# Performance work log

Hardware: AMD Instinct MI355X
Metric: run time of the kernel (lower is better)

Reference implementation:

```python
import jax, jax.numpy as jnp
import numpy as np

N_SIGMA = 1
NUM_CLASS = 1
N_INST = 16          # max instance id (ids 1..16); instances==0 is background
W_INST, W_VAR, W_SEED = 1.0, 10.0, 1.0
H, W, B = 512, 512, 8
GRID = 1024          # buffer is linspace over 1024 then cropped to H,W


def make_xym(h, w, dtype=jnp.float32):
    full = jnp.linspace(0.0, 1.0, GRID, dtype=dtype)
    xm = jnp.broadcast_to(full[:w][None, :], (h, w))   # x varies along width
    ym = jnp.broadcast_to(full[:h][:, None], (h, w))   # y varies along height
    return jnp.stack([xm, ym], axis=0)                 # [2, H, W]


def lovasz_hinge_flat(logits, labels):
    # logits: [N] float, labels: [N] float in {0,1}
    signs = 2.0 * labels - 1.0
    errors = 1.0 - logits * signs
    order = jnp.argsort(-errors)
    errors_sorted = errors[order]
    gt_sorted = labels[order]
    gts = jnp.sum(gt_sorted)
    intersection = gts - jnp.cumsum(gt_sorted)
    union = gts + jnp.cumsum(1.0 - gt_sorted)
    jaccard = 1.0 - intersection / union
    grad = jnp.concatenate([jaccard[:1], jaccard[1:] - jaccard[:-1]])
    return jnp.sum(jax.nn.relu(errors_sorted) * grad)


def _per_image(pred, instance, label, xym):
    h, w = pred.shape[1], pred.shape[2]
    spatial_emb = jnp.tanh(pred[0:2]) + xym              # [2,H,W]
    sigma = pred[2:2 + N_SIGMA]                          # [n_sigma,H,W]
    seed = jax.nn.sigmoid(pred[2 + N_SIGMA])             # [H,W] (num_class==1)

    label_mask = (label == 1)
    bg_mask = (label == 0)
    seed_loss = jnp.sum(jnp.where(bg_mask, seed ** 2, 0.0))

    ids = jnp.arange(1, N_INST + 1)
    masks = (instance[None] == ids[:, None, None]) & label_mask[None]  # [K,H,W] bool
    maskf = masks.astype(pred.dtype)
    counts = jnp.sum(maskf, axis=(1, 2))                 # [K]
    present = counts > 0
    safe = jnp.maximum(counts, 1.0)

    # to_center=True: center = mean of xym coords over each instance mask
    center = jnp.einsum('khw,chw->kc', maskf, xym) / safe[:, None]        # [K,2]
    s_mean = jnp.einsum('khw,shw->ks', maskf, sigma) / safe[:, None]      # [K,n_sigma]

    # var loss: mean over in-mask pixels of (sigma - detached mean)^2
    dev2 = (sigma[None] - jax.lax.stop_gradient(s_mean)[:, :, None, None]) ** 2  # [K,ns,H,W]
    var_terms = jnp.einsum('khw,kshw->k', maskf, dev2) / (safe * N_SIGMA)

    # dist = exp(-s * sum_c (emb_c - center_c)^2), s = exp(10 * mean sigma)
    s_exp = jnp.exp(10.0 * s_mean)[:, 0]                 # [K] (n_sigma==1 broadcasts)
    diff2 = jnp.sum((spatial_emb[None] - center[:, :, None, None]) ** 2, axis=1)  # [K,H,W]
    dist = jnp.exp(-s_exp[:, None, None] * diff2)        # [K,H,W]

    inst_losses = jax.vmap(
        lambda d, m: lovasz_hinge_flat(2.0 * d.ravel() - 1.0, m.ravel())
    )(dist, maskf)
    instance_loss = jnp.sum(jnp.where(present, inst_losses, 0.0))
    var_loss = jnp.sum(jnp.where(present, var_terms, 0.0))

    seed_loss = seed_loss + jnp.sum(
        maskf * (seed[None] - jax.lax.stop_gradient(dist)) ** 2)

    obj = jnp.maximum(jnp.sum(present.astype(pred.dtype)), 1.0)
    return (W_INST * instance_loss / obj
            + W_VAR * var_loss / obj
            + W_SEED * seed_loss / (h * w))


def setup_inputs() -> dict:
    key = jax.random.key(0)
    k1, k2, k3 = jax.random.split(key, 3)
    prediction = jax.random.normal(k1, (B, 2 + N_SIGMA + NUM_CLASS, H, W), dtype=jnp.float32)
    instances = jax.random.randint(k2, (B, H, W), 0, N_INST + 1).astype(jnp.int64)
    labels = jax.random.randint(k3, (B, H, W), 0, NUM_CLASS + 1).astype(jnp.int64)
    return {"prediction": prediction, "instances": instances, "labels": labels}


def reference(prediction, instances, labels):
    xym = make_xym(prediction.shape[2], prediction.shape[3], prediction.dtype)
    per_img = jax.vmap(_per_image, in_axes=(0, 0, 0, None))(
        prediction, instances, labels, xym)
    return jnp.mean(per_img)
```

## Files before the change

kernel.cpp:

```cpp
#include <hip/hip_runtime.h>
#include <math.h>

#define HWPX 262144
#define NIMG 8
#define ACC_STRIDE 96
#define NB 512
#define ZMAX 8.0f
#define NSPLIT 64
#define PREP_GRID 2048

typedef unsigned long long u64;

__device__ __forceinline__ float tanh_fast(float x) {
  float t = __expf(2.0f * x);
  return 1.0f - __fdividef(2.0f, t + 1.0f);
}
__device__ __forceinline__ float sigmoid_fast(float x) {
  return __fdividef(1.0f, 1.0f + __expf(-x));
}

__global__ __launch_bounds__(256) void k_stats(const float* __restrict__ pred,
    const int* __restrict__ inst, const int* __restrict__ lab,
    float* __restrict__ part)
{
  __shared__ float s[8][83];
  int t = threadIdx.x;
  for (int i = t; i < 8*83; i += 256) (&s[0][0])[i] = 0.0f;
  __syncthreads();
  int bid = blockIdx.x;
  int b = bid >> 8;
  int px0 = ((bid & 255) << 10) + t*4;
  const float* pb = pred + (size_t)b*4*HWPX;
  size_t ib = (size_t)b*HWPX;
  int r = t & 7;
  int w0 = px0 & 511;
  float ym = (float)(px0 >> 9) * (1.0f/1023.0f);

  float4 Gv = *(const float4*)(pb + 2*HWPX + px0);
  float4 Q  = *(const float4*)(pb + 3*HWPX + px0);
  int4   L  = *(const int4*)(lab + ib + px0);
  int4   I  = *(const int4*)(inst + ib + px0);

  float bg = 0.0f;
#define PXS(C, GG, QQ, LL, II) { \
    float xm = (float)(w0 + C) * (1.0f/1023.0f); \
    int mid = ((LL) == 1 && (unsigned)((II)-1) < 16u) ? (II) : 0; \
    if ((LL) == 0) { float sd = sigmoid_fast(QQ); bg += sd*sd; } \
    else if (mid) { int k = mid - 1; \
      atomicAdd(&s[r][k], 1.0f); \
      atomicAdd(&s[r][16+k], xm); \
      atomicAdd(&s[r][32+k], ym); \
      atomicAdd(&s[r][48+k], GG); \
      atomicAdd(&s[r][64+k], (GG)*(GG)); } }
  PXS(0, Gv.x, Q.x, L.x, I.x)
  PXS(1, Gv.y, Q.y, L.y, I.y)
  PXS(2, Gv.z, Q.z, L.z, I.z)
  PXS(3, Gv.w, Q.w, L.w, I.w)
#undef PXS

  #pragma unroll
  for (int o = 32; o > 0; o >>= 1) bg += __shfl_down(bg, o);
  if ((t & 63) == 0) atomicAdd(&s[0][80], bg);
  __syncthreads();
  if (t < 96) {
    float v = 0.0f;
    if (t < 83) {
      #pragma unroll
      for (int rr = 0; rr < 8; ++rr) v += s[rr][t];
    }
    part[(size_t)bid*96 + t] = v;
  }
}

__global__ __launch_bounds__(1024) void k_fin(const float* __restrict__ part,
    double* __restrict__ accd, float* __restrict__ pairinfo)
{
  __shared__ float red2[10*96];
  int t = threadIdx.x, b = blockIdx.x;
  if (t < 960) {
    int e = t % 96, c = t / 96;
    int lo = c*26, hi = lo + 26; if (hi > 256) hi = 256;
    const float* pp = part + (size_t)b*256*96 + e;
    float v = 0.0f;
    for (int blk = lo; blk < hi; ++blk) v += pp[(size_t)blk*96];
    red2[c*96 + e] = v;
  }
  __syncthreads();
  if (t < 96) {
    float v = 0.0f;
    #pragma unroll
    for (int cc = 0; cc < 10; ++cc) v += red2[cc*96 + t];
    red2[t] = v;
  }
  __syncthreads();
  if (t < 16) {
    float cnt = red2[t];
    float safe = cnt > 0.0f ? cnt : 1.0f;
    float sm = red2[48+t] / safe;
    float4 pi = make_float4(red2[16+t]/safe, red2[32+t]/safe, __expf(10.0f*sm), cnt);
    ((float4*)pairinfo)[b*16 + t] = pi;
  }
  if (t == 0) {
    double vs = 0.0; float np = 0.0f;
    for (int k2 = 0; k2 < 16; ++k2) {
      float cnt = red2[k2];
      if (cnt > 0.0f) {
        np += 1.0f;
        float ssg = red2[48+k2];
        float var = (red2[64+k2] - ssg*ssg/cnt) / cnt;
        if (var < 0.0f) var = 0.0f;
        vs += (double)var;
      }
    }
    double* ab = accd + (size_t)b*ACC_STRIDE;
    ab[80] = (double)red2[80];
    ab[81] = 0.0;
    ab[82] = 0.0;
    ab[83] = vs;
    ab[84] = np > 1.0f ? (double)np : 1.0;
  }
}

__global__ __launch_bounds__(1024, 4) void k_hist(const float* __restrict__ pred,
    const int* __restrict__ inst, const int* __restrict__ lab,
    const float* __restrict__ pairinfo,
    unsigned* __restrict__ partial, double* __restrict__ accd)
{
  __shared__ unsigned hist[16*NB];
  __shared__ float redf[16];
  int t = threadIdx.x, bid = blockIdx.x;
  int b = bid & 7;
  int s = bid >> 3;
  for (int i = t; i < 16*NB; i += 1024) hist[i] = 0u;
  float cx[16], cy[16], s128[16];
  #pragma unroll
  for (int j = 0; j < 16; ++j) {
    float4 pi = ((const float4*)pairinfo)[b*16 + j];
    cx[j] = pi.x; cy[j] = pi.y; s128[j] = pi.z * (float)(NB/ZMAX);
  }
  __syncthreads();
  int px0 = s*(HWPX/NSPLIT) + t*4;
  const float* pb = pred + (size_t)b*4*HWPX;
  size_t ib = (size_t)b*HWPX;
  float4 X = *(const float4*)(pb + px0);
  float4 Y = *(const float4*)(pb + HWPX + px0);
  float4 Q = *(const float4*)(pb + 3*HWPX + px0);
  int4   L = *(const int4*)(lab + ib + px0);
  int4   I = *(const int4*)(inst + ib + px0);
  int w0 = px0 & 511;
  float ym = (float)(px0 >> 9) * (1.0f/1023.0f);
  float fit = 0.0f;

#define PXH(C, XX, YY, QQ, LL, II) { \
    float xm = (float)(w0 + C) * (1.0f/1023.0f); \
    float exf = tanh_fast(XX) + xm; \
    float eyf = tanh_fast(YY) + ym; \
    float sd = sigmoid_fast(QQ); \
    int rel = ((LL) == 1 && (unsigned)((II)-1) < 16u) ? ((II)-1) : -1; \
    _Pragma("unroll") \
    for (int j = 0; j < 16; ++j) { \
      float dx = exf - cx[j], dy = eyf - cy[j]; \
      float z = fmaf(dx, dx, dy*dy) * s128[j]; \
      float d = __expf(-z * (ZMAX/(float)NB)); \
      bool m = (j == rel); \
      float e = fmaf(-2.0f, d, 2.0f); \
      int kp = (int)(e * (float)(NB/2)); kp = kp > NB-1 ? NB-1 : kp; \
      int kn = (int)fminf(z, (float)(NB-1)); \
      atomicAdd(&hist[j*NB + (m ? kp : kn)], m ? 0x10000u : 1u); \
      if (m) { float df = sd - d; fit += df*df; } \
    } }
  PXH(0, X.x, Y.x, Q.x, L.x, I.x)
  PXH(1, X.y, Y.y, Q.y, L.y, I.y)
  PXH(2, X.z, Y.z, Q.z, L.z, I.z)
  PXH(3, X.w, Y.w, Q.w, L.w, I.w)
#undef PXH

  #pragma unroll
  for (int o = 32; o > 0; o >>= 1) fit += __shfl_down(fit, o);
  if ((t & 63) == 0) redf[t >> 6] = fit;
  __syncthreads();
  if (t == 0) {
    float ft = 0.0f;
    for (int i = 0; i < 16; ++i) ft += redf[i];
    atomicAdd(&accd[(size_t)b*ACC_STRIDE + 81], (double)ft);
  }
  unsigned* pp = partial + (size_t)(b*NSPLIT + s)*(16*NB);
  for (int i = t; i < 16*NB; i += 1024) pp[i] = hist[i];
}

__global__ __launch_bounds__(512) void k_scan(const unsigned* __restrict__ partial,
    const float* __restrict__ pairinfo, double* __restrict__ accd)
{
  __shared__ unsigned sp[NB], sq[NB];
  __shared__ float red[8];
  int t = threadIdx.x, bid = blockIdx.x;
  int b = bid >> 4, k = bid & 15;
  float G = pairinfo[(b*16 + k)*4 + 3];
  if (G <= 0.0f) return;
  sq[t] = 0u;
  __syncthreads();
  unsigned p = 0, q = 0;
  const unsigned* basep = partial + (size_t)(b*NSPLIT)*(16*NB) + k*NB + t;
  #pragma unroll 4
  for (int s2 = 0; s2 < NSPLIT; ++s2) {
    unsigned h = basep[(size_t)s2*(16*NB)];
    p += h >> 16; q += h & 0xffffu;
  }
  float zmid = (t + 0.5f) * (ZMAX/NB);
  float ev = 2.0f * __expf(-zmid);
  int eb = (int)(ev * (float)(NB/2));
  if (eb > NB-1) eb = NB-1;
  if (q) atomicAdd(&sq[eb], q);
  __syncthreads();
  unsigned qe = sq[t];
  __syncthreads();
  int j = (NB-1) - t;
  sp[j] = p; sq[j] = qe;
  __syncthreads();
  for (int off = 1; off < NB; off <<= 1) {
    unsigned vp = 0, vq = 0;
    if (j >= off) { vp = sp[j-off]; vq = sq[j-off]; }
    __syncthreads();
    sp[j] += vp; sq[j] += vq;
    __syncthreads();
  }
  float A  = (float)(sp[j] - p);
  float Bn = (float)(sq[j] - qe);
  float val = (t + 0.5f) * (2.0f/NB);
  float pf = (float)p, qf = (float)qe;
  float Jb = (A + Bn) / (G + Bn);
  float Ja = (A + Bn + pf + qf) / (G + Bn + qf);
  float contrib = val * (Ja - Jb);
  #pragma unroll
  for (int o = 32; o > 0; o >>= 1) contrib += __shfl_down(contrib, o);
  if ((t & 63) == 0) red[t >> 6] = contrib;
  __syncthreads();
  if (t == 0) {
    float tot = 0.0f;
    for (int i = 0; i < 8; ++i) tot += red[i];
    atomicAdd(&accd[(size_t)b*ACC_STRIDE + 82], (double)tot);
  }
}

__global__ __launch_bounds__(1024) void k_lov_old(const float* __restrict__ pred,
    const int* __restrict__ inst, const int* __restrict__ lab,
    const float* __restrict__ pairinfo, double* __restrict__ accd)
{
  constexpr int SHIFT = 18;
  constexpr int NBB = (0x40000000 >> SHIFT) + 1;
  extern __shared__ unsigned char smem[];
  unsigned* histP = reinterpret_cast<unsigned*>(smem);
  unsigned* histQ = histP + NBB;
  unsigned* scanP = histQ + NBB;
  unsigned* scanQ = scanP + 1024;
  float* red  = reinterpret_cast<float*>(scanQ + 1024);
  float* redf = red + 16;
  int t = threadIdx.x, bid = blockIdx.x;
  int b = bid >> 4, k = bid & 15;
  float4 pi = reinterpret_cast<const float4*>(pairinfo)[bid];
  float cx = pi.x, cy = pi.y, sexp = pi.z, G = pi.w;
  if (G <= 0.0f) return;
  for (int i = t; i < 2*NBB; i += 1024) histP[i] = 0u;
  __syncthreads();
  size_t ib = (size_t)b * HWPX;
  const float* pb = pred + (size_t)b * 4 * HWPX;
  const int target = k + 1;
  float fit = 0.0f;
  for (int j = 0; j < HWPX/1024; ++j) {
    int px = (j << 10) + t;
    int h = px >> 9, w = px & 511;
    float ex = tanhf(pb[px]) + w*(1.0f/1023.0f);
    float ey = tanhf(pb[HWPX+px]) + h*(1.0f/1023.0f);
    float sd = 1.0f/(1.0f + __expf(-pb[3*HWPX+px]));
    int lv = lab[ib+px], iv = inst[ib+px];
    float dx = ex - cx, dy = ey - cy;
    float d = __expf(-sexp * (dx*dx + dy*dy));
    bool m = (lv == 1) && (iv == target);
    float e = m ? fmaf(-2.0f, d, 2.0f) : 2.0f * d;
    unsigned key = __float_as_uint(e) >> SHIFT;
    atomicAdd(m ? &histP[key] : &histQ[key], 1u);
    if (m) { float df = sd - d; fit += df*df; }
  }
  #pragma unroll
  for (int o = 32; o > 0; o >>= 1) fit += __shfl_down(fit, o);
  if ((t & 63) == 0) redf[t >> 6] = fit;
  __syncthreads();
  constexpr int CB = NBB / 1024;
  int start = (NBB - 1) - t * CB;
  int nk = (t == 1023) ? (CB + 1) : CB;
  unsigned lp = 0, lq = 0;
  for (int i = 0; i < nk; ++i) { lp += histP[start-i]; lq += histQ[start-i]; }
  scanP[t] = lp; scanQ[t] = lq;
  __syncthreads();
  for (int off = 1; off < 1024; off <<= 1) {
    unsigned vp = 0, vq = 0;
    if (t >= off) { vp = scanP[t-off]; vq = scanQ[t-off]; }
    __syncthreads();
    scanP[t] += vp; scanQ[t] += vq;
    __syncthreads();
  }
  float A  = (float)(scanP[t] - lp);
  float Bn = (float)(scanQ[t] - lq);
  float contrib = 0.0f;
  for (int i = 0; i < nk; ++i) {
    int kk = start - i;
    unsigned p = histP[kk], q = histQ[kk];
    if (p | q) {
      float lo = __uint_as_float((unsigned)kk << SHIFT);
      float hi = __uint_as_float((unsigned)(kk+1) << SHIFT);
      float valv = 0.5f*(lo+hi);
      if (valv > 2.0f) valv = 2.0f;
      float pq = (float)(p + q), qf = (float)q;
      float Jb = (A + Bn) / (G + Bn);
      float Ja = (A + Bn + pq) / (G + Bn + qf);
      contrib += valv * (Ja - Jb);
      A += (float)p; Bn += qf;
    }
  }
  #pragma unroll
  for (int o = 32; o > 0; o >>= 1) contrib += __shfl_down(contrib, o);
  if ((t & 63) == 0) red[t >> 6] = contrib;
  __syncthreads();
  if (t == 0) {
    float tot = 0.0f, ft = 0.0f;
    for (int i = 0; i < 16; ++i) { tot += red[i]; ft += redf[i]; }
    atomicAdd(&accd[(size_t)b*ACC_STRIDE + 82], (double)tot);
    atomicAdd(&accd[(size_t)b*ACC_STRIDE + 81], (double)ft);
  }
}

__global__ void k_final(const double* __restrict__ accd, float* __restrict__ out)
{
  int t = threadIdx.x;
  double lb = 0.0;
  if (t < NIMG) {
    const double* ab = accd + (size_t)t*ACC_STRIDE;
    lb = (ab[82] + 10.0*ab[83]) / ab[84] + (ab[80] + ab[81]) * (1.0/(double)HWPX);
  }
  #pragma unroll
  for (int o = 4; o > 0; o >>= 1) lb += __shfl_down(lb, o);
  if (t == 0) out[0] = (float)(lb * 0.125);
}

extern "C" void kernel_launch(void* const* d_in, const int* in_sizes, int n_in,
                              void* d_out, int out_size, void* d_ws, size_t ws_size,
                              hipStream_t stream)
{
  const float* pred = (const float*)d_in[0];
  const int*   inst = (const int*)d_in[1];
  const int*   lab  = (const int*)d_in[2];
  float* out = (float*)d_out;

  size_t partB  = (size_t)NIMG * NSPLIT * 16 * NB * 4;
  size_t pstatB = (size_t)PREP_GRID * 96 * sizeof(float);
  size_t accB   = (size_t)NIMG * ACC_STRIDE * sizeof(double);
  size_t pairB  = 128 * 4 * sizeof(float);
  bool full = ws_size >= partB + pstatB + accB + pairB;

  char* ws = (char*)d_ws;
  if (full) {
    unsigned* part  = (unsigned*)ws;
    float*    pstat = (float*)(ws + partB);
    double*   accd  = (double*)(ws + partB + pstatB);
    float*    pairinfo = (float*)(ws + partB + pstatB + accB);
    k_stats<<<PREP_GRID,256,0,stream>>>(pred, inst, lab, pstat);
    k_fin<<<NIMG,1024,0,stream>>>(pstat, accd, pairinfo);
    k_hist<<<NIMG*NSPLIT,1024,0,stream>>>(pred, inst, lab, pairinfo, part, accd);
    k_scan<<<128,512,0,stream>>>(part, pairinfo, accd);
    k_final<<<1,64,0,stream>>>(accd, out);
  } else {
    float*    pstat = (float*)ws;
    double*   accd  = (double*)(ws + pstatB);
    float*    pairinfo = (float*)(ws + pstatB + accB);
    k_stats<<<PREP_GRID,256,0,stream>>>(pred, inst, lab, pstat);
    k_fin<<<NIMG,1024,0,stream>>>(pstat, accd, pairinfo);
    size_t lds18 = ((size_t)2*4097 + 2048)*4 + 128;
    k_lov_old<<<128,1024,lds18,stream>>>(pred, inst, lab, pairinfo, accd);
    k_final<<<1,64,0,stream>>>(accd, out);
  }
}
```

Before: 81.75 us.

## Pack seed and instance id in stats pass, slim histogram kernel, fuse final reduction

The stats kernel now writes a packed per-pixel word holding the fp16 seed sigmoid and the valid instance id. The histogram kernel reads that word instead of the seed, label and instance arrays. The histogram kernel uses 256-thread blocks that each process 16 pixels per thread, and it evaluates the exponential only for the pixel's own instance. The final reduction moves into the scan kernel through a last-block ticket counter, which removes one launch. This adds an 8 MB intermediate write, fp16 rounding of the seed value, and reliance on the ticket counter's initial state.

```diff
diff --git a/kernel.cpp b/kernel.cpp
--- a/kernel.cpp
+++ b/kernel.cpp
@@ -1,4 +1,5 @@
 #include <hip/hip_runtime.h>
+#include <hip/hip_fp16.h>
 #include <math.h>
 
 #define HWPX 262144
@@ -7,7 +8,7 @@
 #define NB 512
 #define ZMAX 8.0f
 #define NSPLIT 64
-#define PREP_GRID 2048
+#define STAT_GRID 2048
 
 typedef unsigned long long u64;
 
@@ -19,9 +20,10 @@
   return __fdividef(1.0f, 1.0f + __expf(-x));
 }
 
+template<bool PACK>
 __global__ __launch_bounds__(256) void k_stats(const float* __restrict__ pred,
     const int* __restrict__ inst, const int* __restrict__ lab,
-    float* __restrict__ part)
+    unsigned* __restrict__ meta, float* __restrict__ part)
 {
   __shared__ float s[8][83];
   int t = threadIdx.x;
@@ -42,21 +44,27 @@
   int4   I  = *(const int4*)(inst + ib + px0);
 
   float bg = 0.0f;
-#define PXS(C, GG, QQ, LL, II) { \
+  unsigned m0=0,m1=0,m2=0,m3=0;
+#define PXS(MV, C, GG, QQ, LL, II) { \
     float xm = (float)(w0 + C) * (1.0f/1023.0f); \
+    float sd = sigmoid_fast(QQ); \
     int mid = ((LL) == 1 && (unsigned)((II)-1) < 16u) ? (II) : 0; \
-    if ((LL) == 0) { float sd = sigmoid_fast(QQ); bg += sd*sd; } \
+    if (PACK) MV = ((unsigned)__half_as_ushort(__float2half(sd)) << 16) | (unsigned)mid; \
+    if ((LL) == 0) { bg += sd*sd; } \
     else if (mid) { int k = mid - 1; \
       atomicAdd(&s[r][k], 1.0f); \
       atomicAdd(&s[r][16+k], xm); \
       atomicAdd(&s[r][32+k], ym); \
       atomicAdd(&s[r][48+k], GG); \
       atomicAdd(&s[r][64+k], (GG)*(GG)); } }
-  PXS(0, Gv.x, Q.x, L.x, I.x)
-  PXS(1, Gv.y, Q.y, L.y, I.y)
-  PXS(2, Gv.z, Q.z, L.z, I.z)
-  PXS(3, Gv.w, Q.w, L.w, I.w)
+  PXS(m0, 0, Gv.x, Q.x, L.x, I.x)
+  PXS(m1, 1, Gv.y, Q.y, L.y, I.y)
+  PXS(m2, 2, Gv.z, Q.z, L.z, I.z)
+  PXS(m3, 3, Gv.w, Q.w, L.w, I.w)
 #undef PXS
+  if (PACK) {
+    *(uint4*)(meta + ib + px0) = make_uint4(m0, m1, m2, m3);
+  }
 
   #pragma unroll
   for (int o = 32; o > 0; o >>= 1) bg += __shfl_down(bg, o);
@@ -121,124 +129,154 @@
   }
 }
 
-__global__ __launch_bounds__(1024, 4) void k_hist(const float* __restrict__ pred,
-    const int* __restrict__ inst, const int* __restrict__ lab,
-    const float* __restrict__ pairinfo,
+__global__ __launch_bounds__(256) void k_hist(const float* __restrict__ pred,
+    const unsigned* __restrict__ meta, const float* __restrict__ pairinfo,
     unsigned* __restrict__ partial, double* __restrict__ accd)
 {
   __shared__ unsigned hist[16*NB];
-  __shared__ float redf[16];
+  __shared__ float redf[4];
   int t = threadIdx.x, bid = blockIdx.x;
   int b = bid & 7;
   int s = bid >> 3;
-  for (int i = t; i < 16*NB; i += 1024) hist[i] = 0u;
+  for (int i = t; i < 16*NB; i += 256) hist[i] = 0u;
   float cx[16], cy[16], s128[16];
   #pragma unroll
   for (int j = 0; j < 16; ++j) {
     float4 pi = ((const float4*)pairinfo)[b*16 + j];
-    cx[j] = pi.x; cy[j] = pi.y; s128[j] = pi.z * (float)(NB/ZMAX);
-  }
-  __syncthreads();
-  int px0 = s*(HWPX/NSPLIT) + t*4;
+    cx[j] = pi.x; cy[j] = pi.y; s128[j] = pi.z * ((float)NB/ZMAX);
+  }
+  __syncthreads();
+  int px0 = s*(HWPX/NSPLIT) + t*16;
   const float* pb = pred + (size_t)b*4*HWPX;
   size_t ib = (size_t)b*HWPX;
-  float4 X = *(const float4*)(pb + px0);
-  float4 Y = *(const float4*)(pb + HWPX + px0);
-  float4 Q = *(const float4*)(pb + 3*HWPX + px0);
-  int4   L = *(const int4*)(lab + ib + px0);
-  int4   I = *(const int4*)(inst + ib + px0);
-  int w0 = px0 & 511;
+  int wbase = px0 & 511;
   float ym = (float)(px0 >> 9) * (1.0f/1023.0f);
   float fit = 0.0f;
 
-#define PXH(C, XX, YY, QQ, LL, II) { \
-    float xm = (float)(w0 + C) * (1.0f/1023.0f); \
+  for (int it4 = 0; it4 < 4; ++it4) {
+    int px = px0 + it4*4;
+    float4 X = *(const float4*)(pb + px);
+    float4 Y = *(const float4*)(pb + HWPX + px);
+    uint4  M = *(const uint4*)(meta + ib + px);
+    int wb = wbase + it4*4;
+#define PXH(C, XX, YY, MM) { \
+    float xm = (float)(wb + C) * (1.0f/1023.0f); \
     float exf = tanh_fast(XX) + xm; \
     float eyf = tanh_fast(YY) + ym; \
-    float sd = sigmoid_fast(QQ); \
-    int rel = ((LL) == 1 && (unsigned)((II)-1) < 16u) ? ((II)-1) : -1; \
+    int rel = (int)((MM) & 0xffu) - 1; \
+    float sd = __half2float(__ushort_as_half((unsigned short)((MM) >> 16))); \
     _Pragma("unroll") \
     for (int j = 0; j < 16; ++j) { \
       float dx = exf - cx[j], dy = eyf - cy[j]; \
       float z = fmaf(dx, dx, dy*dy) * s128[j]; \
-      float d = __expf(-z * (ZMAX/(float)NB)); \
-      bool m = (j == rel); \
-      float e = fmaf(-2.0f, d, 2.0f); \
-      int kp = (int)(e * (float)(NB/2)); kp = kp > NB-1 ? NB-1 : kp; \
-      int kn = (int)fminf(z, (float)(NB-1)); \
-      atomicAdd(&hist[j*NB + (m ? kp : kn)], m ? 0x10000u : 1u); \
-      if (m) { float df = sd - d; fit += df*df; } \
+      int key; unsigned add; \
+      if (j == rel) { \
+        float d = __expf(-z * (ZMAX/(float)NB)); \
+        float e = fmaf(-2.0f, d, 2.0f); \
+        int kp = (int)(e * (float)(NB/2)); key = kp > NB-1 ? NB-1 : kp; \
+        add = 0x10000u; \
+        float df = sd - d; fit += df*df; \
+      } else { \
+        key = (int)fminf(z, (float)(NB-1)); \
+        add = 1u; \
+      } \
+      atomicAdd(&hist[j*NB + key], add); \
     } }
-  PXH(0, X.x, Y.x, Q.x, L.x, I.x)
-  PXH(1, X.y, Y.y, Q.y, L.y, I.y)
-  PXH(2, X.z, Y.z, Q.z, L.z, I.z)
-  PXH(3, X.w, Y.w, Q.w, L.w, I.w)
+    PXH(0, X.x, Y.x, M.x)
+    PXH(1, X.y, Y.y, M.y)
+    PXH(2, X.z, Y.z, M.z)
+    PXH(3, X.w, Y.w, M.w)
 #undef PXH
+  }
 
   #pragma unroll
   for (int o = 32; o > 0; o >>= 1) fit += __shfl_down(fit, o);
   if ((t & 63) == 0) redf[t >> 6] = fit;
   __syncthreads();
   if (t == 0) {
-    float ft = 0.0f;
-    for (int i = 0; i < 16; ++i) ft += redf[i];
+    float ft = redf[0] + redf[1] + redf[2] + redf[3];
     atomicAdd(&accd[(size_t)b*ACC_STRIDE + 81], (double)ft);
   }
   unsigned* pp = partial + (size_t)(b*NSPLIT + s)*(16*NB);
-  for (int i = t; i < 16*NB; i += 1024) pp[i] = hist[i];
+  for (int i = t; i < 16*NB; i += 256) pp[i] = hist[i];
 }
 
 __global__ __launch_bounds__(512) void k_scan(const unsigned* __restrict__ partial,
-    const float* __restrict__ pairinfo, double* __restrict__ accd)
+    const float* __restrict__ pairinfo, double* __restrict__ accd,
+    float* __restrict__ out, unsigned* __restrict__ tick)
 {
   __shared__ unsigned sp[NB], sq[NB];
   __shared__ float red[8];
+  __shared__ int lastFlag;
   int t = threadIdx.x, bid = blockIdx.x;
   int b = bid >> 4, k = bid & 15;
   float G = pairinfo[(b*16 + k)*4 + 3];
-  if (G <= 0.0f) return;
-  sq[t] = 0u;
-  __syncthreads();
-  unsigned p = 0, q = 0;
-  const unsigned* basep = partial + (size_t)(b*NSPLIT)*(16*NB) + k*NB + t;
-  #pragma unroll 4
-  for (int s2 = 0; s2 < NSPLIT; ++s2) {
-    unsigned h = basep[(size_t)s2*(16*NB)];
-    p += h >> 16; q += h & 0xffffu;
-  }
-  float zmid = (t + 0.5f) * (ZMAX/NB);
-  float ev = 2.0f * __expf(-zmid);
-  int eb = (int)(ev * (float)(NB/2));
-  if (eb > NB-1) eb = NB-1;
-  if (q) atomicAdd(&sq[eb], q);
-  __syncthreads();
-  unsigned qe = sq[t];
-  __syncthreads();
-  int j = (NB-1) - t;
-  sp[j] = p; sq[j] = qe;
-  __syncthreads();
-  for (int off = 1; off < NB; off <<= 1) {
-    unsigned vp = 0, vq = 0;
-    if (j >= off) { vp = sp[j-off]; vq = sq[j-off]; }
-    __syncthreads();
-    sp[j] += vp; sq[j] += vq;
-    __syncthreads();
-  }
-  float A  = (float)(sp[j] - p);
-  float Bn = (float)(sq[j] - qe);
-  float val = (t + 0.5f) * (2.0f/NB);
-  float pf = (float)p, qf = (float)qe;
-  float Jb = (A + Bn) / (G + Bn);
-  float Ja = (A + Bn + pf + qf) / (G + Bn + qf);
-  float contrib = val * (Ja - Jb);
-  #pragma unroll
-  for (int o = 32; o > 0; o >>= 1) contrib += __shfl_down(contrib, o);
-  if ((t & 63) == 0) red[t >> 6] = contrib;
-  __syncthreads();
+  if (G > 0.0f) {
+    sq[t] = 0u;
+    __syncthreads();
+    unsigned p = 0, q = 0;
+    const unsigned* basep = partial + (size_t)(b*NSPLIT)*(16*NB) + k*NB + t;
+    #pragma unroll 4
+    for (int s2 = 0; s2 < NSPLIT; ++s2) {
+      unsigned h = basep[(size_t)s2*(16*NB)];
+      p += h >> 16; q += h & 0xffffu;
+    }
+    float zmid = (t + 0.5f) * (ZMAX/NB);
+    float ev = 2.0f * __expf(-zmid);
+    int eb = (int)(ev * (float)(NB/2));
+    if (eb > NB-1) eb = NB-1;
+    if (q) atomicAdd(&sq[eb], q);
+    __syncthreads();
+    unsigned qe = sq[t];
+    __syncthreads();
+    int j = (NB-1) - t;
+    sp[j] = p; sq[j] = qe;
+    __syncthreads();
+    for (int off = 1; off < NB; off <<= 1) {
+      unsigned vp = 0, vq = 0;
+      if (j >= off) { vp = sp[j-off]; vq = sq[j-off]; }
+      __syncthreads();
+      sp[j] += vp; sq[j] += vq;
+      __syncthreads();
+    }
+    float A  = (float)(sp[j] - p);
+    float Bn = (float)(sq[j] - qe);
+    float val = (t + 0.5f) * (2.0f/NB);
+    float pf = (float)p, qf = (float)qe;
+    float Jb = (A + Bn) / (G + Bn);
+    float Ja = (A + Bn + pf + qf) / (G + Bn + qf);
+    float contrib = val * (Ja - Jb);
+    #pragma unroll
+    for (int o = 32; o > 0; o >>= 1) contrib += __shfl_down(contrib, o);
+    if ((t & 63) == 0) red[t >> 6] = contrib;
+    __syncthreads();
+    if (t == 0) {
+      float tot = 0.0f;
+      for (int i = 0; i < 8; ++i) tot += red[i];
+      atomicAdd(&accd[(size_t)b*ACC_STRIDE + 82], (double)tot);
+    }
+  }
   if (t == 0) {
-    float tot = 0.0f;
-    for (int i = 0; i < 8; ++i) tot += red[i];
-    atomicAdd(&accd[(size_t)b*ACC_STRIDE + 82], (double)tot);
+    __threadfence();
+    unsigned old = atomicAdd(tick, 1u);
+    lastFlag = ((old & 127u) == 127u) ? 1 : 0;
+  }
+  __syncthreads();
+  if (!lastFlag) return;
+  double lb = 0.0;
+  if (t < NIMG) {
+    double* ab = accd + (size_t)t*ACC_STRIDE;
+    double v80 = atomicAdd(&ab[80], 0.0);
+    double v81 = atomicAdd(&ab[81], 0.0);
+    double v82 = atomicAdd(&ab[82], 0.0);
+    double v83 = atomicAdd(&ab[83], 0.0);
+    double v84 = atomicAdd(&ab[84], 0.0);
+    lb = (v82 + 10.0*v83) / v84 + (v80 + v81) * (1.0/(double)HWPX);
+  }
+  if (t < 64) {
+    #pragma unroll
+    for (int o = 4; o > 0; o >>= 1) lb += __shfl_down(lb, o);
+    if (t == 0) out[0] = (float)(lb * 0.125);
   }
 }
 
@@ -351,28 +389,31 @@
   const int*   lab  = (const int*)d_in[2];
   float* out = (float*)d_out;
 
+  size_t metaB  = (size_t)NIMG * HWPX * 4;
   size_t partB  = (size_t)NIMG * NSPLIT * 16 * NB * 4;
-  size_t pstatB = (size_t)PREP_GRID * 96 * sizeof(float);
+  size_t pstatB = (size_t)STAT_GRID * 96 * sizeof(float);
   size_t accB   = (size_t)NIMG * ACC_STRIDE * sizeof(double);
   size_t pairB  = 128 * 4 * sizeof(float);
-  bool full = ws_size >= partB + pstatB + accB + pairB;
+  size_t tickB  = 64;
+  bool full = ws_size >= metaB + partB + pstatB + accB + pairB + tickB;
 
   char* ws = (char*)d_ws;
   if (full) {
-    unsigned* part  = (unsigned*)ws;
-    float*    pstat = (float*)(ws + partB);
-    double*   accd  = (double*)(ws + partB + pstatB);
-    float*    pairinfo = (float*)(ws + partB + pstatB + accB);
-    k_stats<<<PREP_GRID,256,0,stream>>>(pred, inst, lab, pstat);
+    unsigned* meta  = (unsigned*)ws;
+    unsigned* part  = (unsigned*)(ws + metaB);
+    float*    pstat = (float*)(ws + metaB + partB);
+    double*   accd  = (double*)(ws + metaB + partB + pstatB);
+    float*    pairinfo = (float*)(ws + metaB + partB + pstatB + accB);
+    unsigned* tick  = (unsigned*)(ws + metaB + partB + pstatB + accB + pairB);
+    k_stats<true><<<STAT_GRID,256,0,stream>>>(pred, inst, lab, meta, pstat);
     k_fin<<<NIMG,1024,0,stream>>>(pstat, accd, pairinfo);
-    k_hist<<<NIMG*NSPLIT,1024,0,stream>>>(pred, inst, lab, pairinfo, part, accd);
-    k_scan<<<128,512,0,stream>>>(part, pairinfo, accd);
-    k_final<<<1,64,0,stream>>>(accd, out);
+    k_hist<<<NIMG*NSPLIT,256,0,stream>>>(pred, meta, pairinfo, part, accd);
+    k_scan<<<128,512,0,stream>>>(part, pairinfo, accd, out, tick);
   } else {
     float*    pstat = (float*)ws;
     double*   accd  = (double*)(ws + pstatB);
     float*    pairinfo = (float*)(ws + pstatB + accB);
-    k_stats<<<PREP_GRID,256,0,stream>>>(pred, inst, lab, pstat);
+    k_stats<false><<<STAT_GRID,256,0,stream>>>(pred, inst, lab, nullptr, pstat);
     k_fin<<<NIMG,1024,0,stream>>>(pstat, accd, pairinfo);
     size_t lds18 = ((size_t)2*4097 + 2048)*4 + 128;
     k_lov_old<<<128,1024,lds18,stream>>>(pred, inst, lab, pairinfo, accd);
```

New measurement: 84.04 us. +2.8%, slower.

## Halve histogram bins, merge partial histograms via global atomics, move bg loss into hist

Applied to the files above, without the earlier changes.

Cuts the Lovasz histogram resolution from 512 to 256 bins. Per-block partial histograms are no longer written out for k_scan to reduce; nonzero bins are atomically added into per-image P/Q arrays that k_fin zeroes, so k_scan reads one value per bin. The background seed term moves from k_stats into k_hist, which avoids reading the seed channel twice, and the hist bin key is computed under a branch so the exp runs only for the matching instance. Coarser bins add approximation error to the Lovasz term, and the global atomics may contend.

```diff
diff --git a/kernel.cpp b/kernel.cpp
--- a/kernel.cpp
+++ b/kernel.cpp
@@ -4,10 +4,10 @@
 #define HWPX 262144
 #define NIMG 8
 #define ACC_STRIDE 96
-#define NB 512
+#define NB 256
 #define ZMAX 8.0f
 #define NSPLIT 64
-#define PREP_GRID 2048
+#define STAT_GRID 2048
 
 typedef unsigned long long u64;
 
@@ -37,34 +37,28 @@
   float ym = (float)(px0 >> 9) * (1.0f/1023.0f);
 
   float4 Gv = *(const float4*)(pb + 2*HWPX + px0);
-  float4 Q  = *(const float4*)(pb + 3*HWPX + px0);
   int4   L  = *(const int4*)(lab + ib + px0);
   int4   I  = *(const int4*)(inst + ib + px0);
 
-  float bg = 0.0f;
-#define PXS(C, GG, QQ, LL, II) { \
-    float xm = (float)(w0 + C) * (1.0f/1023.0f); \
+#define PXS(C, GG, LL, II) { \
     int mid = ((LL) == 1 && (unsigned)((II)-1) < 16u) ? (II) : 0; \
-    if ((LL) == 0) { float sd = sigmoid_fast(QQ); bg += sd*sd; } \
-    else if (mid) { int k = mid - 1; \
+    if (mid) { int k = mid - 1; \
+      float xm = (float)(w0 + C) * (1.0f/1023.0f); \
       atomicAdd(&s[r][k], 1.0f); \
       atomicAdd(&s[r][16+k], xm); \
       atomicAdd(&s[r][32+k], ym); \
       atomicAdd(&s[r][48+k], GG); \
       atomicAdd(&s[r][64+k], (GG)*(GG)); } }
-  PXS(0, Gv.x, Q.x, L.x, I.x)
-  PXS(1, Gv.y, Q.y, L.y, I.y)
-  PXS(2, Gv.z, Q.z, L.z, I.z)
-  PXS(3, Gv.w, Q.w, L.w, I.w)
+  PXS(0, Gv.x, L.x, I.x)
+  PXS(1, Gv.y, L.y, I.y)
+  PXS(2, Gv.z, L.z, I.z)
+  PXS(3, Gv.w, L.w, I.w)
 #undef PXS
 
-  #pragma unroll
-  for (int o = 32; o > 0; o >>= 1) bg += __shfl_down(bg, o);
-  if ((t & 63) == 0) atomicAdd(&s[0][80], bg);
   __syncthreads();
   if (t < 96) {
     float v = 0.0f;
-    if (t < 83) {
+    if (t < 80) {
       #pragma unroll
       for (int rr = 0; rr < 8; ++rr) v += s[rr][t];
     }
@@ -73,10 +67,15 @@
 }
 
 __global__ __launch_bounds__(1024) void k_fin(const float* __restrict__ part,
-    double* __restrict__ accd, float* __restrict__ pairinfo)
+    double* __restrict__ accd, float* __restrict__ pairinfo,
+    unsigned* __restrict__ Pg, unsigned* __restrict__ Qg)
 {
   __shared__ float red2[10*96];
   int t = threadIdx.x, b = blockIdx.x;
+  for (int i = t; i < 16*NB; i += 1024) {
+    Pg[b*16*NB + i] = 0u;
+    Qg[b*16*NB + i] = 0u;
+  }
   if (t < 960) {
     int e = t % 96, c = t / 96;
     int lo = c*26, hi = lo + 26; if (hi > 256) hi = 256;
@@ -113,7 +112,7 @@
       }
     }
     double* ab = accd + (size_t)b*ACC_STRIDE;
-    ab[80] = (double)red2[80];
+    ab[80] = 0.0;
     ab[81] = 0.0;
     ab[82] = 0.0;
     ab[83] = vs;
@@ -121,13 +120,13 @@
   }
 }
 
-__global__ __launch_bounds__(1024, 4) void k_hist(const float* __restrict__ pred,
+__global__ __launch_bounds__(1024) void k_hist(const float* __restrict__ pred,
     const int* __restrict__ inst, const int* __restrict__ lab,
     const float* __restrict__ pairinfo,
-    unsigned* __restrict__ partial, double* __restrict__ accd)
+    unsigned* __restrict__ Pg, unsigned* __restrict__ Qg, double* __restrict__ accd)
 {
   __shared__ unsigned hist[16*NB];
-  __shared__ float redf[16];
+  __shared__ float redf[16], redb[16];
   int t = threadIdx.x, bid = blockIdx.x;
   int b = bid & 7;
   int s = bid >> 3;
@@ -136,7 +135,7 @@
   #pragma unroll
   for (int j = 0; j < 16; ++j) {
     float4 pi = ((const float4*)pairinfo)[b*16 + j];
-    cx[j] = pi.x; cy[j] = pi.y; s128[j] = pi.z * (float)(NB/ZMAX);
+    cx[j] = pi.x; cy[j] = pi.y; s128[j] = pi.z * ((float)NB/ZMAX);
   }
   __syncthreads();
   int px0 = s*(HWPX/NSPLIT) + t*4;
@@ -149,7 +148,7 @@
   int4   I = *(const int4*)(inst + ib + px0);
   int w0 = px0 & 511;
   float ym = (float)(px0 >> 9) * (1.0f/1023.0f);
-  float fit = 0.0f;
+  float fit = 0.0f, bg = 0.0f;
 
 #define PXH(C, XX, YY, QQ, LL, II) { \
     float xm = (float)(w0 + C) * (1.0f/1023.0f); \
@@ -157,17 +156,23 @@
     float eyf = tanh_fast(YY) + ym; \
     float sd = sigmoid_fast(QQ); \
     int rel = ((LL) == 1 && (unsigned)((II)-1) < 16u) ? ((II)-1) : -1; \
+    bg += ((LL) == 0) ? sd*sd : 0.0f; \
     _Pragma("unroll") \
     for (int j = 0; j < 16; ++j) { \
       float dx = exf - cx[j], dy = eyf - cy[j]; \
       float z = fmaf(dx, dx, dy*dy) * s128[j]; \
-      float d = __expf(-z * (ZMAX/(float)NB)); \
-      bool m = (j == rel); \
-      float e = fmaf(-2.0f, d, 2.0f); \
-      int kp = (int)(e * (float)(NB/2)); kp = kp > NB-1 ? NB-1 : kp; \
-      int kn = (int)fminf(z, (float)(NB-1)); \
-      atomicAdd(&hist[j*NB + (m ? kp : kn)], m ? 0x10000u : 1u); \
-      if (m) { float df = sd - d; fit += df*df; } \
+      int key; unsigned add; \
+      if (j == rel) { \
+        float d = __expf(-z * (ZMAX/(float)NB)); \
+        float e = fmaf(-2.0f, d, 2.0f); \
+        int kp = (int)(e * (float)(NB/2)); key = kp > NB-1 ? NB-1 : kp; \
+        add = 0x10000u; \
+        float df = sd - d; fit += df*df; \
+      } else { \
+        key = (int)fminf(z, (float)(NB-1)); \
+        add = 1u; \
+      } \
+      atomicAdd(&hist[j*NB + key], add); \
     } }
   PXH(0, X.x, Y.x, Q.x, L.x, I.x)
   PXH(1, X.y, Y.y, Q.y, L.y, I.y)
@@ -176,36 +181,39 @@
 #undef PXH
 
   #pragma unroll
-  for (int o = 32; o > 0; o >>= 1) fit += __shfl_down(fit, o);
-  if ((t & 63) == 0) redf[t >> 6] = fit;
+  for (int o = 32; o > 0; o >>= 1) { fit += __shfl_down(fit, o); bg += __shfl_down(bg, o); }
+  if ((t & 63) == 0) { redf[t >> 6] = fit; redb[t >> 6] = bg; }
   __syncthreads();
   if (t == 0) {
-    float ft = 0.0f;
-    for (int i = 0; i < 16; ++i) ft += redf[i];
+    float ft = 0.0f, bt = 0.0f;
+    for (int i = 0; i < 16; ++i) { ft += redf[i]; bt += redb[i]; }
     atomicAdd(&accd[(size_t)b*ACC_STRIDE + 81], (double)ft);
-  }
-  unsigned* pp = partial + (size_t)(b*NSPLIT + s)*(16*NB);
-  for (int i = t; i < 16*NB; i += 1024) pp[i] = hist[i];
-}
-
-__global__ __launch_bounds__(512) void k_scan(const unsigned* __restrict__ partial,
+    atomicAdd(&accd[(size_t)b*ACC_STRIDE + 80], (double)bt);
+  }
+  for (int i = t; i < 16*NB; i += 1024) {
+    unsigned h = hist[i];
+    if (h) {
+      unsigned hp = h >> 16, hq = h & 0xffffu;
+      if (hp) atomicAdd(&Pg[b*16*NB + i], hp);
+      if (hq) atomicAdd(&Qg[b*16*NB + i], hq);
+    }
+  }
+}
+
+__global__ __launch_bounds__(NB) void k_scan(const unsigned* __restrict__ Pg,
+    const unsigned* __restrict__ Qg,
     const float* __restrict__ pairinfo, double* __restrict__ accd)
 {
   __shared__ unsigned sp[NB], sq[NB];
-  __shared__ float red[8];
+  __shared__ float red[4];
   int t = threadIdx.x, bid = blockIdx.x;
   int b = bid >> 4, k = bid & 15;
   float G = pairinfo[(b*16 + k)*4 + 3];
   if (G <= 0.0f) return;
   sq[t] = 0u;
   __syncthreads();
-  unsigned p = 0, q = 0;
-  const unsigned* basep = partial + (size_t)(b*NSPLIT)*(16*NB) + k*NB + t;
-  #pragma unroll 4
-  for (int s2 = 0; s2 < NSPLIT; ++s2) {
-    unsigned h = basep[(size_t)s2*(16*NB)];
-    p += h >> 16; q += h & 0xffffu;
-  }
+  unsigned p = Pg[(b*16 + k)*NB + t];
+  unsigned q = Qg[(b*16 + k)*NB + t];
   float zmid = (t + 0.5f) * (ZMAX/NB);
   float ev = 2.0f * __expf(-zmid);
   int eb = (int)(ev * (float)(NB/2));
@@ -236,10 +244,49 @@
   if ((t & 63) == 0) red[t >> 6] = contrib;
   __syncthreads();
   if (t == 0) {
-    float tot = 0.0f;
-    for (int i = 0; i < 8; ++i) tot += red[i];
+    float tot = red[0] + red[1] + red[2] + red[3];
     atomicAdd(&accd[(size_t)b*ACC_STRIDE + 82], (double)tot);
   }
+}
+
+__global__ void k_final(const double* __restrict__ accd, float* __restrict__ out)
+{
+  int t = threadIdx.x;
+  double lb = 0.0;
+  if (t < NIMG) {
+    const double* ab = accd + (size_t)t*ACC_STRIDE;
+    lb = (ab[82] + 10.0*ab[83]) / ab[84] + (ab[80] + ab[81]) * (1.0/(double)HWPX);
+  }
+  #pragma unroll
+  for (int o = 4; o > 0; o >>= 1) lb += __shfl_down(lb, o);
+  if (t == 0) out[0] = (float)(lb * 0.125);
+}
+
+__global__ __launch_bounds__(256) void k_bg(const float* __restrict__ pred,
+    const int* __restrict__ lab, double* __restrict__ accd)
+{
+  __shared__ float redb[4];
+  int t = threadIdx.x, bid = blockIdx.x;
+  int b = bid >> 8;
+  int px0 = ((bid & 255) << 10) + t*4;
+  const float* pb = pred + (size_t)b*4*HWPX;
+  size_t ib = (size_t)b*HWPX;
+  float4 Q = *(const float4*)(pb + 3*HWPX + px0);
+  int4   L = *(const int4*)(lab + ib + px0);
+  float bg = 0.0f;
+  float qs[4] = {Q.x,Q.y,Q.z,Q.w};
+  int   ls[4] = {L.x,L.y,L.z,L.w};
+  #pragma unroll
+  for (int c = 0; c < 4; ++c) {
+    float sd = sigmoid_fast(qs[c]);
+    bg += (ls[c] == 0) ? sd*sd : 0.0f;
+  }
+  #pragma unroll
+  for (int o = 32; o > 0; o >>= 1) bg += __shfl_down(bg, o);
+  if ((t & 63) == 0) redb[t >> 6] = bg;
+  __syncthreads();
+  if (t == 0) atomicAdd(&accd[(size_t)b*ACC_STRIDE + 80],
+                        (double)(redb[0]+redb[1]+redb[2]+redb[3]));
 }
 
 __global__ __launch_bounds__(1024) void k_lov_old(const float* __restrict__ pred,
@@ -329,19 +376,6 @@
   }
 }
 
-__global__ void k_final(const double* __restrict__ accd, float* __restrict__ out)
-{
-  int t = threadIdx.x;
-  double lb = 0.0;
-  if (t < NIMG) {
-    const double* ab = accd + (size_t)t*ACC_STRIDE;
-    lb = (ab[82] + 10.0*ab[83]) / ab[84] + (ab[80] + ab[81]) * (1.0/(double)HWPX);
-  }
-  #pragma unroll
-  for (int o = 4; o > 0; o >>= 1) lb += __shfl_down(lb, o);
-  if (t == 0) out[0] = (float)(lb * 0.125);
-}
-
 extern "C" void kernel_launch(void* const* d_in, const int* in_sizes, int n_in,
                               void* d_out, int out_size, void* d_ws, size_t ws_size,
                               hipStream_t stream)
@@ -351,29 +385,33 @@
   const int*   lab  = (const int*)d_in[2];
   float* out = (float*)d_out;
 
-  size_t partB  = (size_t)NIMG * NSPLIT * 16 * NB * 4;
-  size_t pstatB = (size_t)PREP_GRID * 96 * sizeof(float);
+  size_t pqB    = (size_t)NIMG * 16 * NB * 4;
+  size_t pstatB = (size_t)STAT_GRID * 96 * sizeof(float);
   size_t accB   = (size_t)NIMG * ACC_STRIDE * sizeof(double);
   size_t pairB  = 128 * 4 * sizeof(float);
-  bool full = ws_size >= partB + pstatB + accB + pairB;
+  bool full = ws_size >= 2*pqB + pstatB + accB + pairB;
 
   char* ws = (char*)d_ws;
   if (full) {
-    unsigned* part  = (unsigned*)ws;
-    float*    pstat = (float*)(ws + partB);
-    double*   accd  = (double*)(ws + partB + pstatB);
-    float*    pairinfo = (float*)(ws + partB + pstatB + accB);
-    k_stats<<<PREP_GRID,256,0,stream>>>(pred, inst, lab, pstat);
-    k_fin<<<NIMG,1024,0,stream>>>(pstat, accd, pairinfo);
-    k_hist<<<NIMG*NSPLIT,1024,0,stream>>>(pred, inst, lab, pairinfo, part, accd);
-    k_scan<<<128,512,0,stream>>>(part, pairinfo, accd);
+    unsigned* Pg    = (unsigned*)ws;
+    unsigned* Qg    = (unsigned*)(ws + pqB);
+    float*    pstat = (float*)(ws + 2*pqB);
+    double*   accd  = (double*)(ws + 2*pqB + pstatB);
+    float*    pairinfo = (float*)(ws + 2*pqB + pstatB + accB);
+    k_stats<<<STAT_GRID,256,0,stream>>>(pred, inst, lab, pstat);
+    k_fin<<<NIMG,1024,0,stream>>>(pstat, accd, pairinfo, Pg, Qg);
+    k_hist<<<NIMG*NSPLIT,1024,0,stream>>>(pred, inst, lab, pairinfo, Pg, Qg, accd);
+    k_scan<<<128,NB,0,stream>>>(Pg, Qg, pairinfo, accd);
     k_final<<<1,64,0,stream>>>(accd, out);
   } else {
     float*    pstat = (float*)ws;
     double*   accd  = (double*)(ws + pstatB);
     float*    pairinfo = (float*)(ws + pstatB + accB);
-    k_stats<<<PREP_GRID,256,0,stream>>>(pred, inst, lab, pstat);
-    k_fin<<<NIMG,1024,0,stream>>>(pstat, accd, pairinfo);
+    unsigned* Pg = (unsigned*)(ws + pstatB + accB + pairB);
+    unsigned* Qg = Pg + NIMG*16*NB;
+    k_stats<<<STAT_GRID,256,0,stream>>>(pred, inst, lab, pstat);
+    k_fin<<<NIMG,1024,0,stream>>>(pstat, accd, pairinfo, Pg, Qg);
+    k_bg<<<STAT_GRID,256,0,stream>>>(pred, lab, accd);
     size_t lds18 = ((size_t)2*4097 + 2048)*4 + 128;
     k_lov_old<<<128,1024,lds18,stream>>>(pred, inst, lab, pairinfo, accd);
     k_final<<<1,64,0,stream>>>(accd, out);
```

Result: faster. 79.36 us (-2.9%).
